# Kernel tuning notes

Hardware: AMD Instinct MI355X
Metric: run time of the kernel (lower is better)

Reference implementation:

```python
import jax, jax.numpy as jnp
import numpy as np

N, F, H, R, DEG, K = 8192, 64, 128, 3, 32, 32
TEMP = 0.3          # config.edge_temperature
NEG_SLOPE = 0.2     # LeakyReLU slope
EPS_LN = 1e-5
W_THRESH = 1e-6


def setup_inputs() -> dict:
    key = jax.random.key(0)
    ks = jax.random.split(key, 16)
    E = N * DEG
    # each node has DEG outgoing edges so no softmax row is empty (-inf everywhere)
    src = jnp.repeat(jnp.arange(N), DEG)
    tgt = jax.random.randint(ks[0], (E,), 0, N)
    edge_index = jnp.stack([src, tgt]).astype(jnp.int64)
    x = jax.random.normal(ks[1], (N, F), jnp.float32)
    edge_attr = jax.random.normal(ks[2], (E, 3), jnp.float32)
    s = lambda k, sh: jax.random.normal(k, sh, jnp.float32) * 0.05
    D = 2 * F + 3  # edge_input_dim
    params = dict(
        Ws1=s(ks[3], (D, H)), bs1=jnp.zeros(H), ln_g=jnp.ones(H), ln_b=jnp.zeros(H),
        Ws2=s(ks[4], (H, 1)), bs2=jnp.zeros(1),
        Wp=s(ks[5], (D, H)), bp=jnp.zeros(H),
        Wr1=s(ks[6], (F, H)), br1=jnp.zeros(H), Wr2=s(ks[7], (H, R)), br2=jnp.zeros(R),
        Wg1=s(ks[8], (R, H, H // 2)), bg1=jnp.zeros((R, H // 2)),
        Wg2=s(ks[9], (R, H // 2, 1)), bg2=jnp.zeros((R, 1)),
        Wc1=s(ks[10], (F, H)), bc1=jnp.zeros(H), Wc2=s(ks[11], (H, 1)), bc2=jnp.zeros(1),
    )
    return {"x": x, "edge_index": edge_index, "edge_attr": edge_attr, **params}


def reference(x, edge_index, edge_attr,
              Ws1, bs1, ln_g, ln_b, Ws2, bs2, Wp, bp,
              Wr1, br1, Wr2, br2, Wg1, bg1, Wg2, bg2,
              Wc1, bc1, Wc2, bc2):
    src, tgt = edge_index[0], edge_index[1]
    num_nodes = x.shape[0]

    # regime encoder on global mean state
    gs = x.mean(axis=0)
    regime_probs = jax.nn.softmax(jax.nn.relu(gs @ Wr1 + br1) @ Wr2 + br2)  # [R]

    # contagion detector (scalar level)
    contagion_level = jax.nn.sigmoid(jax.nn.relu(x @ Wc1 + bc1) @ Wc2 + bc2).mean()

    # gather -> edge MLP scorer with LayerNorm + LeakyReLU
    edge_input = jnp.concatenate([x[src], x[tgt], edge_attr], axis=-1)  # [E, 2F+3]
    h = edge_input @ Ws1 + bs1
    mu = h.mean(-1, keepdims=True)
    var = h.var(-1, keepdims=True)
    h = (h - mu) * jax.lax.rsqrt(var + EPS_LN) * ln_g + ln_b
    h = jnp.where(h >= 0, h, NEG_SLOPE * h)
    edge_scores_raw = h @ Ws2 + bs2  # [E, 1]

    # regime gating
    edge_hidden = jax.nn.relu(edge_input @ Wp + bp)  # [E, H]
    g1 = jax.nn.relu(jnp.einsum('eh,rhm->erm', edge_hidden, Wg1) + bg1)
    gates = jax.nn.sigmoid(jnp.einsum('erm,rmo->ero', g1, Wg2) + bg2)[..., 0]  # [E, R]
    gate_combined = (gates * regime_probs).sum(-1, keepdims=True)  # [E, 1]

    amp = 1.0 + 0.5 * contagion_level
    edge_scores = (edge_scores_raw * gate_combined * amp)[:, 0]  # [E]

    # scatter into dense NxN, masked softmax per source row, top-k
    M = jnp.full((num_nodes, num_nodes), -jnp.inf, x.dtype).at[src, tgt].set(edge_scores)
    P = jax.nn.softmax(M / TEMP, axis=-1)  # [N, N]
    topk_values, topk_indices = jax.lax.top_k(P, K)  # [N, K]

    # in-device compaction equivalent: weights below threshold zeroed (dropped edges)
    new_edge_weights = jnp.where(topk_values > W_THRESH, topk_values, 0.0)  # [N, K]
    return new_edge_weights, topk_indices
```

## Files before the change

kernel.cpp:

```cpp
#include <hip/hip_runtime.h>
#include <hip/hip_bf16.h>
#include <math.h>

#define NN 8192
#define FF 64
#define HH 128
#define RR 3
#define DEG 32
#define KK 32
#define EE (NN*DEG)
#define DD 131
#define TEMP 0.3f
#define NEG_SLOPE 0.2f
#define EPS_LN 1e-5f
#define W_THRESH 1e-6f

typedef float v2f __attribute__((ext_vector_type(2)));
__device__ __forceinline__ float4 ld4(const float* p) { return *(const float4*)p; }
#define PKFMA(a, b, c) __builtin_elementwise_fma((a), (b), (c))
#define AIDX(a, j) a[((j)>>2)*2 + (((j)&3)>>1)][(j)&1]
#define GIDX(r, g) gaccv[r][(g)>>1][(g)&1]


__global__ __launch_bounds__(256) void stats_kernel(
    const float* __restrict__ x, const float* __restrict__ Wc1,
    const float* __restrict__ bc1, const float* __restrict__ Wc2,
    const float* __restrict__ bc2, float* __restrict__ hdr)
{
    __shared__ float xs[64 * 65];
    __shared__ float wl[64 * 128];
    __shared__ float cs[4][64];
    int t = threadIdx.x;
    int n0 = blockIdx.x * 64;

    for (int i = 0; i < 16; i++) {
        int flat = t + i * 256;
        int r = flat >> 6, c = flat & 63;
        xs[r * 65 + c] = x[(n0 + r) * 64 + c];
    }
    for (int i = 0; i < 32; i++) {
        int flat = t + i * 256;
        wl[flat] = Wc1[flat];
    }
    __syncthreads();

    {
        int col = t & 63, g = t >> 6;
        float ps = 0.f;
        for (int r = g * 16; r < g * 16 + 16; r++) ps += xs[r * 65 + col];
        cs[g][col] = ps;
    }
    __syncthreads();
    if (t < 64) {
        float v = cs[0][t] + cs[1][t] + cs[2][t] + cs[3][t];
        atomicAdd(&hdr[8 + t], v);
    }

    int r = t >> 2, q = t & 3;
    float accl = 0.f;
    for (int hh = 0; hh < 32; hh++) {
        int h = hh * 4 + q;
        float s = bc1[h];
        for (int i = 0; i < 64; i++) s += xs[r * 65 + i] * wl[i * 128 + h];
        accl += fmaxf(s, 0.f) * Wc2[h];
    }
    accl += __shfl_xor(accl, 1);
    accl += __shfl_xor(accl, 2);
    if (q == 0) {
        float lvl = 1.f / (1.f + expf(-(accl + bc2[0])));
        atomicAdd(&hdr[0], lvl);
    }
}

__global__ __launch_bounds__(128) void regime_kernel(
    const float* __restrict__ Wr1, const float* __restrict__ br1,
    const float* __restrict__ Wr2, const float* __restrict__ br2,
    float* __restrict__ hdr)
{
    __shared__ float gsl[64];
    __shared__ float t1[128];
    int t = threadIdx.x;
    if (t < 64) gsl[t] = hdr[8 + t] * (1.f / (float)NN);
    __syncthreads();
    float a = br1[t];
    for (int i = 0; i < 64; i++) a += gsl[i] * Wr1[i * 128 + t];
    t1[t] = fmaxf(a, 0.f);
    __syncthreads();
    if (t < 3) {
        float v = br2[t];
        for (int h = 0; h < 128; h++) v += t1[h] * Wr2[h * 3 + t];
        gsl[32 + t] = v;
    }
    __syncthreads();
    if (t == 0) {
        float v0 = gsl[32], v1 = gsl[33], v2 = gsl[34];
        float m = fmaxf(v0, fmaxf(v1, v2));
        float e0 = expf(v0 - m), e1 = expf(v1 - m), e2 = expf(v2 - m);
        float inv = 1.f / (e0 + e1 + e2);
        hdr[1] = e0 * inv; hdr[2] = e1 * inv; hdr[3] = e2 * inv;
        hdr[4] = 1.f + 0.5f * (hdr[0] * (1.f / (float)NN));
    }
}

__global__ __launch_bounds__(256) void partial_kernel(
    const float* __restrict__ x, const float* __restrict__ Ws1,
    const float* __restrict__ Wp, float* __restrict__ PA)
{
    __shared__ float xs[32 * 65];
    __shared__ float wl[64 * 128];
    int t = threadIdx.x;
    int which = blockIdx.x & 1;
    int n0 = (blockIdx.x >> 1) * 32;
    const float* base = which ? Wp : Ws1;

    for (int i = t; i < 2048; i += 256)
        xs[(i >> 6) * 65 + (i & 63)] = x[n0 * 64 + i];
    for (int it = 0; it < 8; it++) {
        int flat = (t + it * 256) * 4;
        *(float4*)&wl[flat] = ld4(&base[flat]);
    }
    __syncthreads();

    int row = t >> 3, colg = t & 7;
    float acc[16];
    #pragma unroll
    for (int j = 0; j < 16; j++) acc[j] = 0.f;
    const float* xr = &xs[row * 65];
    for (int k = 0; k < 64; k++) {
        float a = xr[k];
        const float* wr = &wl[k * 128 + colg * 16];
        #pragma unroll
        for (int jj = 0; jj < 4; jj++) {
            float4 w = ld4(wr + 4 * jj);
            acc[4*jj+0] += a * w.x; acc[4*jj+1] += a * w.y;
            acc[4*jj+2] += a * w.z; acc[4*jj+3] += a * w.w;
        }
    }
    float* outp = PA + (size_t)which * (NN * 128) + (size_t)(n0 + row) * 128 + colg * 16;
    #pragma unroll
    for (int j = 0; j < 16; j++) outp[j] = acc[j];
}

#define EIB_S 76
#define EHT_S 132
__global__ __launch_bounds__(512) void edge_fused_kernel(
    const int* __restrict__ tgt_idx, const float* __restrict__ edge_attr,
    const float* __restrict__ x,
    const float* __restrict__ Ws1, const float* __restrict__ bs1,
    const float* __restrict__ ln_g, const float* __restrict__ ln_b,
    const float* __restrict__ Ws2, const float* __restrict__ bs2,
    const float* __restrict__ Wp, const float* __restrict__ bp,
    const float* __restrict__ Wg1, const float* __restrict__ bg1,
    const float* __restrict__ Wg2, const float* __restrict__ bg2,
    const float* __restrict__ PA1, const float* __restrict__ PA2,
    const float* __restrict__ hdr,
    float* __restrict__ out_w, float* __restrict__ out_i)
{
    __shared__ float pool[12928];
    __shared__ int   tlS[4][33];
    __shared__ float plS[4][33];
    __shared__ float scrS[128];
    float* EIB   = pool;
    float* WPan  = pool + 9728;
    float* ehTh  = pool;
    float* WgPan = pool + 8448;
    float* Gbuf  = pool;
    float* rawS  = pool + 12800;

    int t = threadIdx.x;
    int e0 = blockIdx.x * 128;

    {
        int r = t >> 2, q = t & 3;
        int ge = e0 + r;
        int tg = tgt_idx[ge];
        #pragma unroll
        for (int i = 0; i < 4; i++) {
            int col = q * 16 + 4 * i;
            *(float4*)&EIB[r * EIB_S + col] = ld4(&x[tg * 64 + col]);
        }
        if (q == 0) {
            float4 v;
            v.x = edge_attr[(size_t)ge * 3 + 0];
            v.y = edge_attr[(size_t)ge * 3 + 1];
            v.z = edge_attr[(size_t)ge * 3 + 2];
            v.w = 0.f;
            *(float4*)&EIB[r * EIB_S + 64] = v;
        } else if (q == 1) {
            *(float4*)&EIB[r * EIB_S + 68] = make_float4(0.f, 0.f, 0.f, 0.f);
        } else if (q == 2) {
            *(float4*)&EIB[r * EIB_S + 72] = make_float4(0.f, 0.f, 0.f, 0.f);
        }
    }

    int tcol = t & 7, trow = t >> 3;
    const float* EIr0 = &EIB[(2 * trow) * EIB_S];
    const float* EIr1 = EIr0 + EIB_S;
    int src = (e0 + 2 * trow) >> 5;

    v2f accs0[8], accs1[8], accp0[8], accp1[8];

    {
        const float* p1 = &PA1[(size_t)src * 128 + tcol * 4];
        const float* p2 = &PA2[(size_t)src * 128 + tcol * 4];
        #pragma unroll
        for (int jj = 0; jj < 4; jj++) {
            float4 v;
            v = ld4(p1 + jj * 32);
            v2f lo1 = { v.x, v.y }, hi1 = { v.z, v.w };
            accs0[jj*2] = lo1; accs0[jj*2+1] = hi1;
            accs1[jj*2] = lo1; accs1[jj*2+1] = hi1;
            v = ld4(p2 + jj * 32);
            v2f lo2 = { v.x, v.y }, hi2 = { v.z, v.w };
            accp0[jj*2] = lo2; accp0[jj*2+1] = hi2;
            accp1[jj*2] = lo2; accp1[jj*2+1] = hi2;
        }
    }

    for (int p = 0; p < 6; p++) {
        __syncthreads();
        #pragma unroll
        for (int i = 0; i < 2; i++) {
            int fid = i * 512 + t;
            if (fid < 768) {
                int mat = (fid >= 384) ? 1 : 0;
                int loc = fid - mat * 384;
                int pr = loc >> 5;
                int pc = (loc & 31) * 4;
                int wrow = 64 + p * 12 + pr;
                const float* Wsrc = mat ? Wp : Ws1;
                float4 w = (wrow < 131) ? ld4(&Wsrc[wrow * 128 + pc])
                                        : make_float4(0.f, 0.f, 0.f, 0.f);
                *(float4*)&WPan[mat * 1536 + pr * 128 + pc] = w;
            }
        }
        __syncthreads();
        for (int kk0 = 0; kk0 < 12; kk0 += 4) {
            float4 a04 = ld4(EIr0 + p * 12 + kk0);
            float4 a14 = ld4(EIr1 + p * 12 + kk0);
            float a0s[4] = { a04.x, a04.y, a04.z, a04.w };
            float a1s[4] = { a14.x, a14.y, a14.z, a14.w };
            #pragma unroll
            for (int u = 0; u < 4; u++) {
                int kk = kk0 + u;
                v2f a0v = { a0s[u], a0s[u] }, a1v = { a1s[u], a1s[u] };
                const float* ws = &WPan[kk * 128 + tcol * 4];
                const float* wq = ws + 1536;
                #pragma unroll
                for (int jj = 0; jj < 4; jj++) {
                    float4 w1 = ld4(ws + jj * 32);
                    v2f w1a = { w1.x, w1.y }, w1b = { w1.z, w1.w };
                    accs0[jj*2]   = PKFMA(a0v, w1a, accs0[jj*2]);
                    accs0[jj*2+1] = PKFMA(a0v, w1b, accs0[jj*2+1]);
                    accs1[jj*2]   = PKFMA(a1v, w1a, accs1[jj*2]);
                    accs1[jj*2+1] = PKFMA(a1v, w1b, accs1[jj*2+1]);
                    float4 w2 = ld4(wq + jj * 32);
                    v2f w2a = { w2.x, w2.y }, w2b = { w2.z, w2.w };
                    accp0[jj*2]   = PKFMA(a0v, w2a, accp0[jj*2]);
                    accp0[jj*2+1] = PKFMA(a0v, w2b, accp0[jj*2+1]);
                    accp1[jj*2]   = PKFMA(a1v, w2a, accp1[jj*2]);
                    accp1[jj*2+1] = PKFMA(a1v, w2b, accp1[jj*2+1]);
                }
            }
        }
    }

    {
        float s0 = 0.f, ss0 = 0.f, s1 = 0.f, ss1 = 0.f;
        #pragma unroll
        for (int j = 0; j < 16; j++) {
            int col = tcol * 4 + (j >> 2) * 32 + (j & 3);
            float b = bs1[col];
            float u0 = AIDX(accs0, j) + b;  AIDX(accs0, j) = u0;
            float u1 = AIDX(accs1, j) + b;  AIDX(accs1, j) = u1;
            s0 += u0; ss0 += u0 * u0;
            s1 += u1; ss1 += u1 * u1;
        }
        #pragma unroll
        for (int m = 1; m < 8; m <<= 1) {
            s0 += __shfl_xor(s0, m);  ss0 += __shfl_xor(ss0, m);
            s1 += __shfl_xor(s1, m);  ss1 += __shfl_xor(ss1, m);
        }
        float mu0 = s0 * (1.f / 128.f), mu1 = s1 * (1.f / 128.f);
        float var0 = ss0 * (1.f / 128.f) - mu0 * mu0;
        float var1 = ss1 * (1.f / 128.f) - mu1 * mu1;
        float inv0 = 1.f / sqrtf(var0 + EPS_LN);
        float inv1 = 1.f / sqrtf(var1 + EPS_LN);
        float d0 = 0.f, d1 = 0.f;
        #pragma unroll
        for (int j = 0; j < 16; j++) {
            int col = tcol * 4 + (j >> 2) * 32 + (j & 3);
            float g = ln_g[col], bb = ln_b[col], w2 = Ws2[col];
            float y0 = (AIDX(accs0, j) - mu0) * inv0 * g + bb;
            float y1 = (AIDX(accs1, j) - mu1) * inv1 * g + bb;
            y0 = (y0 >= 0.f) ? y0 : NEG_SLOPE * y0;
            y1 = (y1 >= 0.f) ? y1 : NEG_SLOPE * y1;
            d0 += y0 * w2; d1 += y1 * w2;
        }
        #pragma unroll
        for (int m = 1; m < 8; m <<= 1) {
            d0 += __shfl_xor(d0, m); d1 += __shfl_xor(d1, m);
        }
        if (tcol == 0) {
            rawS[2 * trow]     = d0 + bs2[0];
            rawS[2 * trow + 1] = d1 + bs2[0];
        }
    }

    int gtr = t >> 4, gtc = t & 15;
    int grow = t >> 2, gq = t & 3;

    v2f gaccv[3][8];
    #pragma unroll
    for (int rr = 0; rr < 3; rr++)
        #pragma unroll
        for (int j = 0; j < 8; j++) gaccv[rr][j] = (v2f){ 0.f, 0.f };

    for (int hf = 0; hf < 2; hf++) {
        __syncthreads();
        #pragma unroll
        for (int j2 = 0; j2 < 8; j2++) {
            int j = hf * 8 + j2;
            int col = tcol * 4 + (j >> 2) * 32 + (j & 3);
            int lc = col - hf * 64;
            float b = bp[col];
            ehTh[lc * EHT_S + 2 * trow]     = fmaxf(AIDX(accp0, j) + b, 0.f);
            ehTh[lc * EHT_S + 2 * trow + 1] = fmaxf(AIDX(accp1, j) + b, 0.f);
        }
        for (int p = 0; p < 4; p++) {
            __syncthreads();
            #pragma unroll
            for (int i = 0; i < 2; i++) {
                int fid = i * 512 + t;
                if (fid < 768) {
                    int rr = fid >> 8;
                    int loc = fid & 255;
                    int pr = loc >> 4;
                    int pc = (loc & 15) * 4;
                    *(float4*)&WgPan[rr * 1024 + pr * 64 + pc] =
                        ld4(&Wg1[(size_t)(rr * 128 + hf * 64 + p * 16 + pr) * 64 + pc]);
                }
            }
            __syncthreads();
            for (int kk = 0; kk < 16; kk++) {
                float4 av = ld4(&ehTh[(p * 16 + kk) * EHT_S + 4 * gtr]);
                v2f ax = { av.x, av.x }, ay = { av.y, av.y };
                v2f az = { av.z, av.z }, aw = { av.w, av.w };
                #pragma unroll
                for (int rr = 0; rr < 3; rr++) {
                    float4 bv = ld4(&WgPan[rr * 1024 + kk * 64 + 4 * gtc]);
                    v2f bva = { bv.x, bv.y }, bvb = { bv.z, bv.w };
                    gaccv[rr][0] = PKFMA(ax, bva, gaccv[rr][0]);
                    gaccv[rr][1] = PKFMA(ax, bvb, gaccv[rr][1]);
                    gaccv[rr][2] = PKFMA(ay, bva, gaccv[rr][2]);
                    gaccv[rr][3] = PKFMA(ay, bvb, gaccv[rr][3]);
                    gaccv[rr][4] = PKFMA(az, bva, gaccv[rr][4]);
                    gaccv[rr][5] = PKFMA(az, bvb, gaccv[rr][5]);
                    gaccv[rr][6] = PKFMA(aw, bva, gaccv[rr][6]);
                    gaccv[rr][7] = PKFMA(aw, bvb, gaccv[rr][7]);
                }
            }
        }
    }

    float gc = 0.f;
    for (int rr = 0; rr < 3; rr++) {
        __syncthreads();
        #pragma unroll
        for (int j = 0; j < 4; j++) {
            float b = bg1[rr * 64 + 4 * gtc + j];
            float4 g;
            g.x = fmaxf(GIDX(rr, 0  + j) + b, 0.f);
            g.y = fmaxf(GIDX(rr, 4  + j) + b, 0.f);
            g.z = fmaxf(GIDX(rr, 8  + j) + b, 0.f);
            g.w = fmaxf(GIDX(rr, 12 + j) + b, 0.f);
            *(float4*)&Gbuf[(4 * gtc + j) * EHT_S + 4 * gtr] = g;
        }
        __syncthreads();
        float pacc = 0.f;
        #pragma unroll
        for (int j = 0; j < 16; j++) {
            int m = gq * 4 + (j >> 2) * 16 + (j & 3);
            pacc += Gbuf[m * EHT_S + grow] * Wg2[rr * 64 + m];
        }
        pacc += __shfl_xor(pacc, 1);
        pacc += __shfl_xor(pacc, 2);
        float gate = 1.f / (1.f + expf(-(pacc + bg2[rr])));
        gc += gate * hdr[1 + rr];
    }
    if (gq == 0) scrS[grow] = rawS[grow] * gc * hdr[4];

    __syncthreads();
    {
        int rowl = t >> 6, j = t & 63;
        bool act = (t < 256) && (j < 32);
        int tg = 0;
        float s = -INFINITY;
        if (act) {
            tg = tgt_idx[e0 + rowl * 32 + j];
            s = scrS[rowl * 32 + j];
            tlS[rowl][j] = tg;
        }
        __syncthreads();
        bool alive = false;
        if (act) {
            alive = true;
            for (int j2 = j + 1; j2 < 32; j2++)
                if (tlS[rowl][j2] == tg) { alive = false; break; }
        }
        float z = (act && alive) ? s * (1.f / TEMP) : -INFINITY;
        float m = z;
        #pragma unroll
        for (int mm = 1; mm < 64; mm <<= 1) m = fmaxf(m, __shfl_xor(m, mm));
        float p = (act && alive) ? expf(z - m) : 0.f;
        float sum = p;
        #pragma unroll
        for (int mm = 1; mm < 64; mm <<= 1) sum += __shfl_xor(sum, mm);
        p = p / sum;
        if (act) plS[rowl][j] = alive ? p : -1.f;
        __syncthreads();

        if (t < 256) {
            int row = blockIdx.x * 4 + rowl;
            int rank = 0, dcount = 0;
            for (int j2 = 0; j2 < 32; j2++) {
                float pj = plS[rowl][j2];
                if (pj >= 0.f) {
                    dcount++;
                    if (act && alive) {
                        if (pj > p || (pj == p && tlS[rowl][j2] < tg)) rank++;
                    }
                }
            }
            if (act && alive) {
                out_w[row * 32 + rank] = (p > W_THRESH) ? p : 0.f;
                out_i[row * 32 + rank] = (float)tg;
            }
            if (j == 0) {
                int c = 0;
                for (int slot = dcount; slot < 32; slot++) {
                    for (;;) {
                        bool found = false;
                        for (int q = 0; q < 32; q++) if (tlS[rowl][q] == c) { found = true; break; }
                        if (!found) break;
                        c++;
                    }
                    out_w[row * 32 + slot] = 0.f;
                    out_i[row * 32 + slot] = (float)c;
                    c++;
                }
            }
        }
    }
}

extern "C" void kernel_launch(void* const* d_in, const int* in_sizes, int n_in,
                              void* d_out, int out_size, void* d_ws, size_t ws_size,
                              hipStream_t stream)
{
    const float* x          = (const float*)d_in[0];
    const int*   edge_index = (const int*)  d_in[1];
    const float* edge_attr  = (const float*)d_in[2];
    const float* Ws1 = (const float*)d_in[3];
    const float* bs1 = (const float*)d_in[4];
    const float* ln_g = (const float*)d_in[5];
    const float* ln_b = (const float*)d_in[6];
    const float* Ws2 = (const float*)d_in[7];
    const float* bs2 = (const float*)d_in[8];
    const float* Wp  = (const float*)d_in[9];
    const float* bp  = (const float*)d_in[10];
    const float* Wr1 = (const float*)d_in[11];
    const float* br1 = (const float*)d_in[12];
    const float* Wr2 = (const float*)d_in[13];
    const float* br2 = (const float*)d_in[14];
    const float* Wg1 = (const float*)d_in[15];
    const float* bg1 = (const float*)d_in[16];
    const float* Wg2 = (const float*)d_in[17];
    const float* bg2 = (const float*)d_in[18];
    const float* Wc1 = (const float*)d_in[19];
    const float* bc1 = (const float*)d_in[20];
    const float* Wc2 = (const float*)d_in[21];
    const float* bc2 = (const float*)d_in[22];

    float* hdr  = (float*)d_ws;
    float* tabs = hdr + 128;
    const int* tgt = edge_index + EE;

    hipMemsetAsync(d_ws, 0, 512, stream);
    stats_kernel<<<128, 256, 0, stream>>>(x, Wc1, bc1, Wc2, bc2, hdr);
    regime_kernel<<<1, 128, 0, stream>>>(Wr1, br1, Wr2, br2, hdr);
    partial_kernel<<<(NN / 32) * 2, 256, 0, stream>>>(x, Ws1, Wp, tabs);
    edge_fused_kernel<<<EE / 128, 512, 0, stream>>>(
        tgt, edge_attr, x, Ws1, bs1, ln_g, ln_b, Ws2, bs2, Wp, bp,
        Wg1, bg1, Wg2, bg2, tabs, tabs + (size_t)NN * 128, hdr,
        (float*)d_out, (float*)d_out + NN * KK);
}
```

Before: 517.2 us.

## Merge stats and partial kernels; halve edge kernel block to 64 edges

After: 477.5 us. 7.7% less time.

```diff
diff --git a/kernel.cpp b/kernel.cpp
--- a/kernel.cpp
+++ b/kernel.cpp
@@ -22,53 +22,93 @@
 #define GIDX(r, g) gaccv[r][(g)>>1][(g)&1]
 
 
-__global__ __launch_bounds__(256) void stats_kernel(
-    const float* __restrict__ x, const float* __restrict__ Wc1,
-    const float* __restrict__ bc1, const float* __restrict__ Wc2,
-    const float* __restrict__ bc2, float* __restrict__ hdr)
+__global__ __launch_bounds__(256) void setup_kernel(
+    const float* __restrict__ x,
+    const float* __restrict__ Ws1, const float* __restrict__ Wp,
+    const float* __restrict__ Wc1, const float* __restrict__ bc1,
+    const float* __restrict__ Wc2, const float* __restrict__ bc2,
+    float* __restrict__ PA, float* __restrict__ hdr)
 {
-    __shared__ float xs[64 * 65];
-    __shared__ float wl[64 * 128];
-    __shared__ float cs[4][64];
+    __shared__ float spool[12608];
     int t = threadIdx.x;
-    int n0 = blockIdx.x * 64;
-
-    for (int i = 0; i < 16; i++) {
-        int flat = t + i * 256;
-        int r = flat >> 6, c = flat & 63;
-        xs[r * 65 + c] = x[(n0 + r) * 64 + c];
-    }
-    for (int i = 0; i < 32; i++) {
-        int flat = t + i * 256;
-        wl[flat] = Wc1[flat];
-    }
-    __syncthreads();
-
-    {
-        int col = t & 63, g = t >> 6;
-        float ps = 0.f;
-        for (int r = g * 16; r < g * 16 + 16; r++) ps += xs[r * 65 + col];
-        cs[g][col] = ps;
-    }
-    __syncthreads();
-    if (t < 64) {
-        float v = cs[0][t] + cs[1][t] + cs[2][t] + cs[3][t];
-        atomicAdd(&hdr[8 + t], v);
-    }
-
-    int r = t >> 2, q = t & 3;
-    float accl = 0.f;
-    for (int hh = 0; hh < 32; hh++) {
-        int h = hh * 4 + q;
-        float s = bc1[h];
-        for (int i = 0; i < 64; i++) s += xs[r * 65 + i] * wl[i * 128 + h];
-        accl += fmaxf(s, 0.f) * Wc2[h];
-    }
-    accl += __shfl_xor(accl, 1);
-    accl += __shfl_xor(accl, 2);
-    if (q == 0) {
-        float lvl = 1.f / (1.f + expf(-(accl + bc2[0])));
-        atomicAdd(&hdr[0], lvl);
+    int bid = blockIdx.x;
+
+    if (bid < 512) {
+        float* xs = spool;
+        float* wl = spool + 2080;
+        int which = bid & 1;
+        int n0 = (bid >> 1) * 32;
+        const float* base = which ? Wp : Ws1;
+
+        for (int i = t; i < 2048; i += 256)
+            xs[(i >> 6) * 65 + (i & 63)] = x[n0 * 64 + i];
+        for (int it = 0; it < 8; it++) {
+            int flat = (t + it * 256) * 4;
+            *(float4*)&wl[flat] = ld4(&base[flat]);
+        }
+        __syncthreads();
+
+        int row = t >> 3, colg = t & 7;
+        float acc[16];
+        #pragma unroll
+        for (int j = 0; j < 16; j++) acc[j] = 0.f;
+        const float* xr = &xs[row * 65];
+        for (int k = 0; k < 64; k++) {
+            float a = xr[k];
+            const float* wr = &wl[k * 128 + colg * 16];
+            #pragma unroll
+            for (int jj = 0; jj < 4; jj++) {
+                float4 w = ld4(wr + 4 * jj);
+                acc[4*jj+0] += a * w.x; acc[4*jj+1] += a * w.y;
+                acc[4*jj+2] += a * w.z; acc[4*jj+3] += a * w.w;
+            }
+        }
+        float* outp = PA + (size_t)which * (NN * 128) + (size_t)(n0 + row) * 128 + colg * 16;
+        #pragma unroll
+        for (int j = 0; j < 16; j++) outp[j] = acc[j];
+    } else {
+        float* xs = spool;
+        float* wl = spool + 4160;
+        float* cs = spool + 12352;
+        int n0 = (bid - 512) * 64;
+
+        for (int i = 0; i < 16; i++) {
+            int flat = t + i * 256;
+            int r = flat >> 6, c = flat & 63;
+            xs[r * 65 + c] = x[(n0 + r) * 64 + c];
+        }
+        for (int i = 0; i < 8; i++) {
+            int flat = (t + i * 256) * 4;
+            *(float4*)&wl[flat] = ld4(&Wc1[flat]);
+        }
+        __syncthreads();
+
+        {
+            int col = t & 63, g = t >> 6;
+            float ps = 0.f;
+            for (int r = g * 16; r < g * 16 + 16; r++) ps += xs[r * 65 + col];
+            cs[g * 64 + col] = ps;
+        }
+        __syncthreads();
+        if (t < 64) {
+            float v = cs[t] + cs[64 + t] + cs[128 + t] + cs[192 + t];
+            atomicAdd(&hdr[8 + t], v);
+        }
+
+        int r = t >> 2, q = t & 3;
+        float accl = 0.f;
+        for (int hh = 0; hh < 32; hh++) {
+            int h = hh * 4 + q;
+            float s = bc1[h];
+            for (int i = 0; i < 64; i++) s += xs[r * 65 + i] * wl[i * 128 + h];
+            accl += fmaxf(s, 0.f) * Wc2[h];
+        }
+        accl += __shfl_xor(accl, 1);
+        accl += __shfl_xor(accl, 2);
+        if (q == 0) {
+            float lvl = 1.f / (1.f + expf(-(accl + bc2[0])));
+            atomicAdd(&hdr[0], lvl);
+        }
     }
 }
 
@@ -102,48 +142,8 @@
     }
 }
 
-__global__ __launch_bounds__(256) void partial_kernel(
-    const float* __restrict__ x, const float* __restrict__ Ws1,
-    const float* __restrict__ Wp, float* __restrict__ PA)
-{
-    __shared__ float xs[32 * 65];
-    __shared__ float wl[64 * 128];
-    int t = threadIdx.x;
-    int which = blockIdx.x & 1;
-    int n0 = (blockIdx.x >> 1) * 32;
-    const float* base = which ? Wp : Ws1;
-
-    for (int i = t; i < 2048; i += 256)
-        xs[(i >> 6) * 65 + (i & 63)] = x[n0 * 64 + i];
-    for (int it = 0; it < 8; it++) {
-        int flat = (t + it * 256) * 4;
-        *(float4*)&wl[flat] = ld4(&base[flat]);
-    }
-    __syncthreads();
-
-    int row = t >> 3, colg = t & 7;
-    float acc[16];
-    #pragma unroll
-    for (int j = 0; j < 16; j++) acc[j] = 0.f;
-    const float* xr = &xs[row * 65];
-    for (int k = 0; k < 64; k++) {
-        float a = xr[k];
-        const float* wr = &wl[k * 128 + colg * 16];
-        #pragma unroll
-        for (int jj = 0; jj < 4; jj++) {
-            float4 w = ld4(wr + 4 * jj);
-            acc[4*jj+0] += a * w.x; acc[4*jj+1] += a * w.y;
-            acc[4*jj+2] += a * w.z; acc[4*jj+3] += a * w.w;
-        }
-    }
-    float* outp = PA + (size_t)which * (NN * 128) + (size_t)(n0 + row) * 128 + colg * 16;
-    #pragma unroll
-    for (int j = 0; j < 16; j++) outp[j] = acc[j];
-}
-
 #define EIB_S 76
-#define EHT_S 132
-__global__ __launch_bounds__(512) void edge_fused_kernel(
+__global__ __launch_bounds__(256) void edge_fused_kernel(
     const int* __restrict__ tgt_idx, const float* __restrict__ edge_attr,
     const float* __restrict__ x,
     const float* __restrict__ Ws1, const float* __restrict__ bs1,
@@ -156,19 +156,19 @@
     const float* __restrict__ hdr,
     float* __restrict__ out_w, float* __restrict__ out_i)
 {
-    __shared__ float pool[12928];
-    __shared__ int   tlS[4][33];
-    __shared__ float plS[4][33];
-    __shared__ float scrS[128];
+    __shared__ float pool[8000];
     float* EIB   = pool;
-    float* WPan  = pool + 9728;
+    float* WPan  = pool + 4864;
     float* ehTh  = pool;
-    float* WgPan = pool + 8448;
+    float* WgPan = pool + 4352;
     float* Gbuf  = pool;
-    float* rawS  = pool + 12800;
+    float* scrS  = pool;
+    int*   tlS   = (int*)(pool + 64);
+    float* plS   = pool + 130;
+    float* rawS  = pool + 7936;
 
     int t = threadIdx.x;
-    int e0 = blockIdx.x * 128;
+    int e0 = blockIdx.x * 64;
 
     {
         int r = t >> 2, q = t & 3;
@@ -220,19 +220,17 @@
     for (int p = 0; p < 6; p++) {
         __syncthreads();
         #pragma unroll
-        for (int i = 0; i < 2; i++) {
-            int fid = i * 512 + t;
-            if (fid < 768) {
-                int mat = (fid >= 384) ? 1 : 0;
-                int loc = fid - mat * 384;
-                int pr = loc >> 5;
-                int pc = (loc & 31) * 4;
-                int wrow = 64 + p * 12 + pr;
-                const float* Wsrc = mat ? Wp : Ws1;
-                float4 w = (wrow < 131) ? ld4(&Wsrc[wrow * 128 + pc])
-                                        : make_float4(0.f, 0.f, 0.f, 0.f);
-                *(float4*)&WPan[mat * 1536 + pr * 128 + pc] = w;
-            }
+        for (int i = 0; i < 3; i++) {
+            int fid = i * 256 + t;
+            int mat = (fid >= 384) ? 1 : 0;
+            int loc = fid - mat * 384;
+            int pr = loc >> 5;
+            int pc = (loc & 31) * 4;
+            int wrow = 64 + p * 12 + pr;
+            const float* Wsrc = mat ? Wp : Ws1;
+            float4 w = (wrow < 131) ? ld4(&Wsrc[wrow * 128 + pc])
+                                    : make_float4(0.f, 0.f, 0.f, 0.f);
+            *(float4*)&WPan[mat * 1536 + pr * 128 + pc] = w;
         }
         __syncthreads();
         for (int kk0 = 0; kk0 < 12; kk0 += 4) {
@@ -324,26 +322,24 @@
             int col = tcol * 4 + (j >> 2) * 32 + (j & 3);
             int lc = col - hf * 64;
             float b = bp[col];
-            ehTh[lc * EHT_S + 2 * trow]     = fmaxf(AIDX(accp0, j) + b, 0.f);
-            ehTh[lc * EHT_S + 2 * trow + 1] = fmaxf(AIDX(accp1, j) + b, 0.f);
+            ehTh[lc * 68 + 2 * trow]     = fmaxf(AIDX(accp0, j) + b, 0.f);
+            ehTh[lc * 68 + 2 * trow + 1] = fmaxf(AIDX(accp1, j) + b, 0.f);
         }
         for (int p = 0; p < 4; p++) {
             __syncthreads();
             #pragma unroll
-            for (int i = 0; i < 2; i++) {
-                int fid = i * 512 + t;
-                if (fid < 768) {
-                    int rr = fid >> 8;
-                    int loc = fid & 255;
-                    int pr = loc >> 4;
-                    int pc = (loc & 15) * 4;
-                    *(float4*)&WgPan[rr * 1024 + pr * 64 + pc] =
-                        ld4(&Wg1[(size_t)(rr * 128 + hf * 64 + p * 16 + pr) * 64 + pc]);
-                }
+            for (int i = 0; i < 3; i++) {
+                int fid = i * 256 + t;
+                int rr = fid >> 8;
+                int loc = fid & 255;
+                int pr = loc >> 4;
+                int pc = (loc & 15) * 4;
+                *(float4*)&WgPan[rr * 1024 + pr * 64 + pc] =
+                    ld4(&Wg1[(size_t)(rr * 128 + hf * 64 + p * 16 + pr) * 64 + pc]);
             }
             __syncthreads();
             for (int kk = 0; kk < 16; kk++) {
-                float4 av = ld4(&ehTh[(p * 16 + kk) * EHT_S + 4 * gtr]);
+                float4 av = ld4(&ehTh[(p * 16 + kk) * 68 + 4 * gtr]);
                 v2f ax = { av.x, av.x }, ay = { av.y, av.y };
                 v2f az = { av.z, av.z }, aw = { av.w, av.w };
                 #pragma unroll
@@ -374,39 +370,39 @@
             g.y = fmaxf(GIDX(rr, 4  + j) + b, 0.f);
             g.z = fmaxf(GIDX(rr, 8  + j) + b, 0.f);
             g.w = fmaxf(GIDX(rr, 12 + j) + b, 0.f);
-            *(float4*)&Gbuf[(4 * gtc + j) * EHT_S + 4 * gtr] = g;
+            *(float4*)&Gbuf[(4 * gtc + j) * 68 + 4 * gtr] = g;
         }
         __syncthreads();
         float pacc = 0.f;
         #pragma unroll
         for (int j = 0; j < 16; j++) {
             int m = gq * 4 + (j >> 2) * 16 + (j & 3);
-            pacc += Gbuf[m * EHT_S + grow] * Wg2[rr * 64 + m];
+            pacc += Gbuf[m * 68 + grow] * Wg2[rr * 64 + m];
         }
         pacc += __shfl_xor(pacc, 1);
         pacc += __shfl_xor(pacc, 2);
         float gate = 1.f / (1.f + expf(-(pacc + bg2[rr])));
         gc += gate * hdr[1 + rr];
     }
-    if (gq == 0) scrS[grow] = rawS[grow] * gc * hdr[4];
-
+
+    __syncthreads();
+    float sc = rawS[grow] * gc * hdr[4];
+    int rowl = t >> 6, j = t & 63;
+    bool act = (rowl < 2) && (j < 32);
+    int tg = 0;
+    if (gq == 0) scrS[grow] = sc;
+    if (act) {
+        tg = tgt_idx[e0 + rowl * 32 + j];
+        tlS[rowl * 33 + j] = tg;
+    }
     __syncthreads();
     {
-        int rowl = t >> 6, j = t & 63;
-        bool act = (t < 256) && (j < 32);
-        int tg = 0;
-        float s = -INFINITY;
-        if (act) {
-            tg = tgt_idx[e0 + rowl * 32 + j];
-            s = scrS[rowl * 32 + j];
-            tlS[rowl][j] = tg;
-        }
-        __syncthreads();
+        float s = act ? scrS[rowl * 32 + j] : -INFINITY;
         bool alive = false;
         if (act) {
             alive = true;
             for (int j2 = j + 1; j2 < 32; j2++)
-                if (tlS[rowl][j2] == tg) { alive = false; break; }
+                if (tlS[rowl * 33 + j2] == tg) { alive = false; break; }
         }
         float z = (act && alive) ? s * (1.f / TEMP) : -INFINITY;
         float m = z;
@@ -417,18 +413,18 @@
         #pragma unroll
         for (int mm = 1; mm < 64; mm <<= 1) sum += __shfl_xor(sum, mm);
         p = p / sum;
-        if (act) plS[rowl][j] = alive ? p : -1.f;
-        __syncthreads();
-
-        if (t < 256) {
-            int row = blockIdx.x * 4 + rowl;
+        if (act) plS[rowl * 33 + j] = alive ? p : -1.f;
+        __syncthreads();
+
+        if (rowl < 2) {
+            int row = blockIdx.x * 2 + rowl;
             int rank = 0, dcount = 0;
             for (int j2 = 0; j2 < 32; j2++) {
-                float pj = plS[rowl][j2];
+                float pj = plS[rowl * 33 + j2];
                 if (pj >= 0.f) {
                     dcount++;
                     if (act && alive) {
-                        if (pj > p || (pj == p && tlS[rowl][j2] < tg)) rank++;
+                        if (pj > p || (pj == p && tlS[rowl * 33 + j2] < tg)) rank++;
                     }
                 }
             }
@@ -441,7 +437,8 @@
                 for (int slot = dcount; slot < 32; slot++) {
                     for (;;) {
                         bool found = false;
-                        for (int q = 0; q < 32; q++) if (tlS[rowl][q] == c) { found = true; break; }
+                        for (int q = 0; q < 32; q++)
+                            if (tlS[rowl * 33 + q] == c) { found = true; break; }
                         if (!found) break;
                         c++;
                     }
@@ -487,10 +484,9 @@
     const int* tgt = edge_index + EE;
 
     hipMemsetAsync(d_ws, 0, 512, stream);
-    stats_kernel<<<128, 256, 0, stream>>>(x, Wc1, bc1, Wc2, bc2, hdr);
+    setup_kernel<<<640, 256, 0, stream>>>(x, Ws1, Wp, Wc1, bc1, Wc2, bc2, tabs, hdr);
     regime_kernel<<<1, 128, 0, stream>>>(Wr1, br1, Wr2, br2, hdr);
-    partial_kernel<<<(NN / 32) * 2, 256, 0, stream>>>(x, Ws1, Wp, tabs);
-    edge_fused_kernel<<<EE / 128, 512, 0, stream>>>(
+    edge_fused_kernel<<<EE / 64, 256, 0, stream>>>(
         tgt, edge_attr, x, Ws1, bs1, ln_g, ln_b, Ws2, bs2, Wp, bp,
         Wg1, bg1, Wg2, bg2, tabs, tabs + (size_t)NN * 128, hdr,
         (float*)d_out, (float*)d_out + NN * KK);
```
